# Kernel optimization log

Hardware: AMD Instinct MI355X
Metric: run time of the kernel (lower is better)

Reference implementation:

```python
import jax, jax.numpy as jnp
import numpy as np

THRESHOLD_FACTOR = 1.25
HIDDEN = 128
B, N = 4, 2048

def setup_inputs() -> dict:
    key = jax.random.key(0)
    ks = jax.random.split(key, 11)
    def lin(k, fin, fout):
        bound = 1.0 / np.sqrt(fin)
        kw, kb = jax.random.split(k)
        W = jax.random.uniform(kw, (fin, fout), jnp.float32, -bound, bound)
        b = jax.random.uniform(kb, (fout,), jnp.float32, -bound, bound)
        return W, b
    W1, b1 = lin(ks[0], 2, HIDDEN)
    W2, b2 = lin(ks[1], HIDDEN, HIDDEN)
    Wd, bd = lin(ks[2], HIDDEN, 1)
    Wr, br = lin(ks[3], HIDDEN, 1)
    Wm, bm = lin(ks[4], HIDDEN, 1)
    phase_coords = jax.random.normal(ks[5], (B, N, 2), jnp.float32)
    return dict(phase_coords=phase_coords, W1=W1, b1=b1, W2=W2, b2=b2,
                Wd=Wd, bd=bd, Wr=Wr, br=br, Wm=Wm, bm=bm)

def _attention(r):
    # diff[b,s,t,i] = r[b,s,i]*(-r[b,t,i]) + r[b,s,i] = r_s * (1 - r_t)
    diff = r[:, :, None, :] * (1.0 - r[:, None, :, :])        # [B,N,N,2]
    dist_sq = jnp.sum(diff * diff, axis=-1)                    # [B,N,N]
    phase_diff = jnp.arctan2(diff[..., 1], diff[..., 0])
    forward_bias = 0.5 * (1.0 + jnp.cos(phase_diff)) * jnp.exp(-dist_sq)
    mean_dist = jnp.mean(dist_sq, axis=(-1, -2), keepdims=True)
    std_dist = jnp.clip(jnp.std(dist_sq, axis=(-1, -2), keepdims=True, ddof=1), 1e-6, None)
    threshold = mean_dist + THRESHOLD_FACTOR * std_dist
    attn = jnp.where(dist_sq <= threshold, forward_bias, 0.0)
    row_sums = jnp.sum(attn, axis=-1, keepdims=True)
    return attn / (row_sums + 1e-8)

def reference(phase_coords, W1, b1, W2, b2, Wd, bd, Wr, br, Wm, bm):
    h = jax.nn.silu(phase_coords @ W1 + b1) @ W2 + b2           # [B,N,H]
    diffusion = h @ Wd + bd                                     # [B,N,1]
    reaction = h @ Wr + br
    migration = h @ Wm + bm
    attn = _attention(phase_coords)                             # [B,N,N]
    diffusion_field = jnp.einsum('bst,btk->bsk', attn, diffusion)
    return diffusion, reaction, migration, attn, diffusion_field
```

## Files before the change

### kernel.cpp

```cpp
#include <hip/hip_runtime.h>
#include <math.h>

#define NTOK 2048
#define HID  128
#define BB   4

typedef float f32x4 __attribute__((ext_vector_type(4)));

__device__ __forceinline__ float wave_red_f(float v) {
  #pragma unroll
  for (int o = 32; o; o >>= 1) v += __shfl_down(v, o, 64);
  return v;
}
__device__ __forceinline__ double wave_red_d(double v) {
  #pragma unroll
  for (int o = 32; o; o >>= 1) v += __shfl_down(v, o, 64);
  return v;
}

__global__ __launch_bounds__(256) void mlp_thr_kernel(
    const float* __restrict__ pc,
    const float* __restrict__ W1, const float* __restrict__ b1,
    const float* __restrict__ W2, const float* __restrict__ b2,
    const float* __restrict__ Wd, const float* __restrict__ bd,
    const float* __restrict__ Wr, const float* __restrict__ br,
    const float* __restrict__ Wm, const float* __restrict__ bm,
    float* __restrict__ outd, float* __restrict__ outr, float* __restrict__ outm,
    float* __restrict__ thr)
{
  const int tid = threadIdx.x;

  if (blockIdx.x >= 32) {
    const int wave = tid >> 6, lane = tid & 63;
    const int b = blockIdx.x - 32;
    const float2* r = (const float2*)(pc + (size_t)b * NTOK * 2);
    double m[10];
    #pragma unroll
    for (int j = 0; j < 10; ++j) m[j] = 0.0;
    for (int i = tid; i < NTOK; i += 256) {
      const float2 c = r[i];
      const double a = c.x, bq = c.y, u = 1.0 - (double)c.x, v = 1.0 - (double)c.y;
      const double a2 = a * a, b2v = bq * bq, u2 = u * u, v2 = v * v;
      m[0] += a2;       m[1] += b2v;
      m[2] += a2 * a2;  m[3] += b2v * b2v;  m[4] += a2 * b2v;
      m[5] += u2;       m[6] += v2;
      m[7] += u2 * u2;  m[8] += v2 * v2;    m[9] += u2 * v2;
    }
    #pragma unroll
    for (int j = 0; j < 10; ++j) m[j] = wave_red_d(m[j]);
    __shared__ double sm[4][10];
    if (lane == 0) {
      #pragma unroll
      for (int j = 0; j < 10; ++j) sm[wave][j] = m[j];
    }
    __syncthreads();
    if (tid == 0) {
      double t[10];
      #pragma unroll
      for (int j = 0; j < 10; ++j)
        t[j] = sm[0][j] + sm[1][j] + sm[2][j] + sm[3][j];
      const double Sq  = t[0] * t[5] + t[1] * t[6];
      const double Sqq = t[2] * t[7] + 2.0 * t[4] * t[9] + t[3] * t[8];
      const double M = (double)NTOK * (double)NTOK;
      const double mean = Sq / M;
      double var = (Sqq - Sq * Sq / M) / (M - 1.0);
      if (var < 0.0) var = 0.0;
      double sd = sqrt(var);
      if (sd < 1e-6) sd = 1e-6;
      thr[b] = (float)(mean + 1.25 * sd);
    }
    return;
  }

  __shared__ float fw[3][HID];
  __shared__ float fc[3];

  for (int idx = tid; idx < 3 * HID; idx += 256) {
    const int head = idx >> 7, k = idx & (HID - 1);
    const float* wh = (head == 0) ? Wd : (head == 1) ? Wr : Wm;
    const float4* w2row = (const float4*)(W2 + k * HID);
    const float4* wh4   = (const float4*)wh;
    float s = 0.f;
    #pragma unroll 4
    for (int j = 0; j < HID / 4; ++j) {
      const float4 a = w2row[j], w = wh4[j];
      s = fmaf(a.x, w.x, fmaf(a.y, w.y, fmaf(a.z, w.z, fmaf(a.w, w.w, s))));
    }
    fw[head][k] = s;
  }
  if (tid < 3) {
    const float* wh = (tid == 0) ? Wd : (tid == 1) ? Wr : Wm;
    const float bh  = (tid == 0) ? bd[0] : (tid == 1) ? br[0] : bm[0];
    const float4* b24 = (const float4*)b2;
    const float4* wh4 = (const float4*)wh;
    float s = 0.f;
    for (int j = 0; j < HID / 4; ++j) {
      const float4 a = b24[j], w = wh4[j];
      s = fmaf(a.x, w.x, fmaf(a.y, w.y, fmaf(a.z, w.z, fmaf(a.w, w.w, s))));
    }
    fc[tid] = s + bh;
  }
  __syncthreads();

  const int row = blockIdx.x * 256 + tid;
  const float2 c = ((const float2*)pc)[row];
  const float x0 = c.x, x1 = c.y;

  float dd = 0.f, rv = 0.f, mv = 0.f;
  #pragma unroll 4
  for (int k = 0; k < HID; ++k) {
    const float z = fmaf(x0, W1[k], fmaf(x1, W1[HID + k], b1[k]));
    const float h = z * __builtin_amdgcn_rcpf(1.f + __builtin_amdgcn_exp2f(-1.442695041f * z));
    dd = fmaf(h, fw[0][k], dd);
    rv = fmaf(h, fw[1][k], rv);
    mv = fmaf(h, fw[2][k], mv);
  }
  outd[row] = dd + fc[0];
  outr[row] = rv + fc[1];
  outm[row] = mv + fc[2];
}

__global__ __launch_bounds__(256) void attn_kernel(
    const float* __restrict__ pc, const float* __restrict__ diffu,
    const float* __restrict__ thr,
    float* __restrict__ attn, float* __restrict__ dfield)
{
  const int b = blockIdx.y;
  const int tid = threadIdx.x, wave = tid >> 6, lane = tid & 63;

  const float2* __restrict__ rr  = (const float2*)(pc + (size_t)b * NTOK * 2);
  const float4* __restrict__ rr4 = (const float4*)rr;
  const float4* __restrict__ sd4 = (const float4*)(diffu + b * NTOK);

  const float C = 1.2011224f;
  float2 u[8];
  float  sdr[8];
  #pragma unroll
  for (int i = 0; i < 2; ++i) {
    const float4 c0 = rr4[tid * 2 + i * 512];
    const float4 c1 = rr4[tid * 2 + 1 + i * 512];
    u[i * 4 + 0] = make_float2(C * (1.f - c0.x), C * (1.f - c0.y));
    u[i * 4 + 1] = make_float2(C * (1.f - c0.z), C * (1.f - c0.w));
    u[i * 4 + 2] = make_float2(C * (1.f - c1.x), C * (1.f - c1.y));
    u[i * 4 + 3] = make_float2(C * (1.f - c1.z), C * (1.f - c1.w));
    const float4 dv = sd4[tid + i * 256];
    sdr[i * 4 + 0] = dv.x; sdr[i * 4 + 1] = dv.y;
    sdr[i * 4 + 2] = dv.z; sdr[i * 4 + 3] = dv.w;
  }

  const float Ts = thr[b] * 1.442695041f;
  const int s0 = blockIdx.x * 4;
  __shared__ float red[2][4][2];

  for (int rs = 0; rs < 4; ++rs) {
    const int s = s0 + rs;
    const float2 rc = rr[s];
    float v[8];
    float rsum = 0.f, dot = 0.f;
    #pragma unroll
    for (int k = 0; k < 8; ++k) {
      const float d0 = rc.x * u[k].x;
      const float d1 = rc.y * u[k].y;
      const float q = fmaf(d0, d0, d1 * d1);
      float val = 0.f;
      if (q <= Ts)
        val = (q > 0.f)
            ? fmaf(d0 * rsqrtf(q), 0.5f, 0.5f) * __builtin_amdgcn_exp2f(-q)
            : 1.f;
      v[k] = val;
      rsum += val;
      dot = fmaf(val, sdr[k], dot);
    }
    rsum = wave_red_f(rsum);
    dot  = wave_red_f(dot);
    if (lane == 0) { red[rs & 1][wave][0] = rsum; red[rs & 1][wave][1] = dot; }
    __syncthreads();
    const float rtot = red[rs & 1][0][0] + red[rs & 1][1][0] +
                       red[rs & 1][2][0] + red[rs & 1][3][0];
    const float dtot = red[rs & 1][0][1] + red[rs & 1][1][1] +
                       red[rs & 1][2][1] + red[rs & 1][3][1];
    const float sc = 1.f / (rtot + 1e-8f);
    f32x4* arow4 = (f32x4*)(attn + ((size_t)b * NTOK + s) * NTOK);
    #pragma unroll
    for (int i = 0; i < 2; ++i) {
      f32x4 o;
      o.x = v[i * 4 + 0] * sc; o.y = v[i * 4 + 1] * sc;
      o.z = v[i * 4 + 2] * sc; o.w = v[i * 4 + 3] * sc;
      arow4[tid + i * 256] = o;
    }
    if (tid == 0) dfield[b * NTOK + s] = dtot * sc;
  }
}

extern "C" void kernel_launch(void* const* d_in, const int* in_sizes, int n_in,
                              void* d_out, int out_size, void* d_ws, size_t ws_size,
                              hipStream_t stream) {
  const float* pc = (const float*)d_in[0];
  const float* W1 = (const float*)d_in[1];
  const float* b1 = (const float*)d_in[2];
  const float* W2 = (const float*)d_in[3];
  const float* b2 = (const float*)d_in[4];
  const float* Wd = (const float*)d_in[5];
  const float* bd = (const float*)d_in[6];
  const float* Wr = (const float*)d_in[7];
  const float* br = (const float*)d_in[8];
  const float* Wm = (const float*)d_in[9];
  const float* bm = (const float*)d_in[10];

  float* out    = (float*)d_out;
  float* outd   = out;
  float* outr   = out + BB * NTOK;
  float* outm   = out + 2 * BB * NTOK;
  float* attn   = out + 3 * BB * NTOK;
  float* dfield = attn + (size_t)BB * NTOK * NTOK;

  float* thr = (float*)d_ws;

  hipLaunchKernelGGL(mlp_thr_kernel, dim3(32 + BB), dim3(256), 0, stream,
                     pc, W1, b1, W2, b2, Wd, bd, Wr, br, Wm, bm,
                     outd, outr, outm, thr);
  hipLaunchKernelGGL(attn_kernel, dim3(NTOK / 4, BB), dim3(256), 0, stream,
                     pc, outd, thr, attn, dfield);
}
```

Measured before the change: 37.04 us.

## Assign one attention row per wavefront and use nontemporal stores

```diff
diff --git a/kernel.cpp b/kernel.cpp
--- a/kernel.cpp
+++ b/kernel.cpp
@@ -126,70 +126,65 @@
     float* __restrict__ attn, float* __restrict__ dfield)
 {
   const int b = blockIdx.y;
-  const int tid = threadIdx.x, wave = tid >> 6, lane = tid & 63;
+  const int wave = threadIdx.x >> 6, lane = threadIdx.x & 63;
+  const int s = blockIdx.x * 4 + wave;
 
   const float2* __restrict__ rr  = (const float2*)(pc + (size_t)b * NTOK * 2);
   const float4* __restrict__ rr4 = (const float4*)rr;
   const float4* __restrict__ sd4 = (const float4*)(diffu + b * NTOK);
 
   const float C = 1.2011224f;
-  float2 u[8];
-  float  sdr[8];
-  #pragma unroll
-  for (int i = 0; i < 2; ++i) {
-    const float4 c0 = rr4[tid * 2 + i * 512];
-    const float4 c1 = rr4[tid * 2 + 1 + i * 512];
-    u[i * 4 + 0] = make_float2(C * (1.f - c0.x), C * (1.f - c0.y));
-    u[i * 4 + 1] = make_float2(C * (1.f - c0.z), C * (1.f - c0.w));
-    u[i * 4 + 2] = make_float2(C * (1.f - c1.x), C * (1.f - c1.y));
-    u[i * 4 + 3] = make_float2(C * (1.f - c1.z), C * (1.f - c1.w));
-    const float4 dv = sd4[tid + i * 256];
-    sdr[i * 4 + 0] = dv.x; sdr[i * 4 + 1] = dv.y;
-    sdr[i * 4 + 2] = dv.z; sdr[i * 4 + 3] = dv.w;
+  float2 u[32];
+  float  sdr[32];
+  #pragma unroll
+  for (int j = 0; j < 8; ++j) {
+    const float4 c0 = rr4[lane * 2 + j * 128];
+    const float4 c1 = rr4[lane * 2 + 1 + j * 128];
+    u[j * 4 + 0] = make_float2(C * (1.f - c0.x), C * (1.f - c0.y));
+    u[j * 4 + 1] = make_float2(C * (1.f - c0.z), C * (1.f - c0.w));
+    u[j * 4 + 2] = make_float2(C * (1.f - c1.x), C * (1.f - c1.y));
+    u[j * 4 + 3] = make_float2(C * (1.f - c1.z), C * (1.f - c1.w));
+    const float4 dv = sd4[lane + j * 64];
+    sdr[j * 4 + 0] = dv.x; sdr[j * 4 + 1] = dv.y;
+    sdr[j * 4 + 2] = dv.z; sdr[j * 4 + 3] = dv.w;
   }
 
   const float Ts = thr[b] * 1.442695041f;
-  const int s0 = blockIdx.x * 4;
-  __shared__ float red[2][4][2];
-
-  for (int rs = 0; rs < 4; ++rs) {
-    const int s = s0 + rs;
-    const float2 rc = rr[s];
-    float v[8];
-    float rsum = 0.f, dot = 0.f;
-    #pragma unroll
-    for (int k = 0; k < 8; ++k) {
-      const float d0 = rc.x * u[k].x;
-      const float d1 = rc.y * u[k].y;
-      const float q = fmaf(d0, d0, d1 * d1);
-      float val = 0.f;
-      if (q <= Ts)
-        val = (q > 0.f)
-            ? fmaf(d0 * rsqrtf(q), 0.5f, 0.5f) * __builtin_amdgcn_exp2f(-q)
-            : 1.f;
-      v[k] = val;
-      rsum += val;
-      dot = fmaf(val, sdr[k], dot);
-    }
-    rsum = wave_red_f(rsum);
-    dot  = wave_red_f(dot);
-    if (lane == 0) { red[rs & 1][wave][0] = rsum; red[rs & 1][wave][1] = dot; }
-    __syncthreads();
-    const float rtot = red[rs & 1][0][0] + red[rs & 1][1][0] +
-                       red[rs & 1][2][0] + red[rs & 1][3][0];
-    const float dtot = red[rs & 1][0][1] + red[rs & 1][1][1] +
-                       red[rs & 1][2][1] + red[rs & 1][3][1];
-    const float sc = 1.f / (rtot + 1e-8f);
-    f32x4* arow4 = (f32x4*)(attn + ((size_t)b * NTOK + s) * NTOK);
-    #pragma unroll
-    for (int i = 0; i < 2; ++i) {
-      f32x4 o;
-      o.x = v[i * 4 + 0] * sc; o.y = v[i * 4 + 1] * sc;
-      o.z = v[i * 4 + 2] * sc; o.w = v[i * 4 + 3] * sc;
-      arow4[tid + i * 256] = o;
-    }
-    if (tid == 0) dfield[b * NTOK + s] = dtot * sc;
-  }
+  const float2 rc = rr[s];
+
+  float v[32];
+  float rsum = 0.f, dot = 0.f;
+  #pragma unroll
+  for (int k = 0; k < 32; ++k) {
+    const float d0 = rc.x * u[k].x;
+    const float d1 = rc.y * u[k].y;
+    const float q = fmaf(d0, d0, d1 * d1);
+    float val = 0.f;
+    if (q <= Ts)
+      val = (q > 0.f)
+          ? fmaf(d0 * rsqrtf(q), 0.5f, 0.5f) * __builtin_amdgcn_exp2f(-q)
+          : 1.f;
+    v[k] = val;
+    rsum += val;
+    dot = fmaf(val, sdr[k], dot);
+  }
+
+  #pragma unroll
+  for (int o = 1; o < 64; o <<= 1) {
+    rsum += __shfl_xor(rsum, o, 64);
+    dot  += __shfl_xor(dot, o, 64);
+  }
+  const float sc = 1.f / (rsum + 1e-8f);
+
+  f32x4* arow4 = (f32x4*)(attn + ((size_t)b * NTOK + s) * NTOK);
+  #pragma unroll
+  for (int j = 0; j < 8; ++j) {
+    f32x4 o;
+    o.x = v[j * 4 + 0] * sc; o.y = v[j * 4 + 1] * sc;
+    o.z = v[j * 4 + 2] * sc; o.w = v[j * 4 + 3] * sc;
+    __builtin_nontemporal_store(o, arow4 + lane + j * 64);
+  }
+  if (lane == 0) dfield[b * NTOK + s] = dot * sc;
 }
 
 extern "C" void kernel_launch(void* const* d_in, const int* in_sizes, int n_in,
```

Measured after the change: 35.90 us. 3.1% less time.
